# Optimization experiments

Measured on AMD Instinct MI355X. Metric: run time of the kernel, lower is better.

## Reference

```python
import jax, jax.numpy as jnp
import numpy as np

BATCH = 2048
NUM_FIELDS = 32
EMBED = 64
NPAIRS = NUM_FIELDS * (NUM_FIELDS - 1) // 2  # 496
# static pair indices (i < j), same order as the torch double loop
ROW, COL = np.triu_indices(NUM_FIELDS, k=1)
ROW = jnp.asarray(ROW)
COL = jnp.asarray(COL)


def setup_inputs() -> dict:
    key = jax.random.key(0)
    k1, k2 = jax.random.split(key)
    emb_inputs = jax.random.normal(k1, (BATCH, NUM_FIELDS, EMBED), dtype=jnp.float32)
    # xavier_normal_ on kernel of shape (E, NC2, E): fan_in = NC2*E (dims[1:]), fan_out = E*E... 
    # torch: fan_in = size(1)*receptive = NPAIRS*EMBED? torch uses size(1)*prod(size[2:]) = NPAIRS*EMBED,
    # fan_out = size(0)*prod(size[2:]) = EMBED*EMBED; std = sqrt(2/(fan_in+fan_out))
    fan_in = NPAIRS * EMBED
    fan_out = EMBED * EMBED
    std = float(np.sqrt(2.0 / (fan_in + fan_out)))
    kernel = jax.random.normal(k2, (EMBED, NPAIRS, EMBED), dtype=jnp.float32) * std
    return {"emb_inputs": emb_inputs, "kernel": kernel}


def reference(emb_inputs, kernel):
    # emb_inputs: (B, N, E); kernel: (E, NC2, E)
    p = emb_inputs[:, ROW]  # (B, NC2, E)
    q = emb_inputs[:, COL]  # (B, NC2, E)
    # torch: kp[b,i,pair] = sum_j p[b,pair,j] * kernel[i,pair,j]; out[b,pair] = sum_i kp*q
    kp = jnp.einsum('bpj,ipj->bpi', p, kernel)  # (B, NC2, E) -- avoids (B,E,NC2,E) blowup
    outputs = jnp.sum(kp * q, axis=-1)          # (B, NC2)
    return outputs[:, None, :]                  # (B, 1, NC2)
```

## Files before the change

### kernel.cpp

```cpp
#include <hip/hip_runtime.h>
#include <hip/hip_bf16.h>

#define BATCH   2048
#define NFIELDS 32
#define EMBED   64
#define NPAIRS  496
#define BT      256

typedef __attribute__((ext_vector_type(8))) short bf16x8;
typedef __attribute__((ext_vector_type(4))) float f32x4;

__device__ __forceinline__ unsigned short f2bf(float x) {
    unsigned int u = __float_as_uint(x);
    unsigned int r = 0x7fffu + ((u >> 16) & 1u);
    return (unsigned short)((u + r) >> 16);
}
__device__ __forceinline__ bf16x8 cvt8(const float* p) {
    float4 v0 = *(const float4*)p;
    float4 v1 = *(const float4*)(p + 4);
    bf16x8 o;
    o[0]=(short)f2bf(v0.x); o[1]=(short)f2bf(v0.y); o[2]=(short)f2bf(v0.z); o[3]=(short)f2bf(v0.w);
    o[4]=(short)f2bf(v1.x); o[5]=(short)f2bf(v1.y); o[6]=(short)f2bf(v1.z); o[7]=(short)f2bf(v1.w);
    return o;
}

__global__ __launch_bounds__(256) void convert_prepass(
    const float* __restrict__ emb, const float* __restrict__ kern,
    unsigned short* __restrict__ embB, unsigned short* __restrict__ kernB)
{
    const int EMB4 = BATCH * NFIELDS * EMBED / 4;
    const int KER4 = EMBED * NPAIRS * EMBED / 4;
    int t = blockIdx.x * blockDim.x + threadIdx.x;
    if (t < EMB4) {
        float4 v = ((const float4*)emb)[t];
        ushort4 o;
        o.x = f2bf(v.x); o.y = f2bf(v.y); o.z = f2bf(v.z); o.w = f2bf(v.w);
        *(ushort4*)(embB + (size_t)t * 4) = o;
    } else if (t < EMB4 + KER4) {
        int u = t - EMB4;
        int j4   = u & 15;
        int rest = u >> 4;
        int p = rest % NPAIRS;
        int i = rest / NPAIRS;
        float4 v = *(const float4*)(kern + (size_t)i * (NPAIRS*EMBED) + (size_t)p * EMBED + j4*4);
        ushort4 o;
        o.x = f2bf(v.x); o.y = f2bf(v.y); o.z = f2bf(v.z); o.w = f2bf(v.w);
        *(ushort4*)(kernB + (size_t)p * 4096 + i * 64 + j4 * 4) = o;
    }
}

template<bool PRE>
__global__ __launch_bounds__(256) void opn_main(
    const void* __restrict__ embP, const void* __restrict__ kernP,
    float* __restrict__ out)
{
    const int pair = blockIdx.x;
    const int bt   = blockIdx.y;

    int r = 0, s0 = 0;
    while (pair >= s0 + (NFIELDS - 1 - r)) { s0 += NFIELDS - 1 - r; ++r; }
    const int c = r + 1 + (pair - s0);

    __shared__ __align__(16) unsigned short Klds[64][72];

    const int tid = threadIdx.x;

    if (PRE) {
        const unsigned short* kb = (const unsigned short*)kernP + (size_t)pair * 4096;
        #pragma unroll
        for (int itk = 0; itk < 2; ++itk) {
            int idx = (itk * 256 + tid) * 8;
            *(bf16x8*)&Klds[idx >> 6][idx & 63] = *(const bf16x8*)(kb + idx);
        }
    } else {
        const float* kf = (const float*)kernP;
        #pragma unroll
        for (int itk = 0; itk < 2; ++itk) {
            int idx = (itk * 256 + tid) * 8;
            int i = idx >> 6, j = idx & 63;
            *(bf16x8*)&Klds[i][j] = cvt8(kf + (size_t)i * (NPAIRS*EMBED) + (size_t)pair * EMBED + j);
        }
    }
    __syncthreads();

    const int wave = tid >> 6, lane = tid & 63;
    const int col = lane & 15, quad = lane >> 4;

    bf16x8 kfr[4][2];
    #pragma unroll
    for (int mt = 0; mt < 4; ++mt)
        #pragma unroll
        for (int ks = 0; ks < 2; ++ks)
            kfr[mt][ks] = *(const bf16x8*)&Klds[mt*16 + col][ks*32 + quad*8];

    const unsigned short* eb = (const unsigned short*)embP;
    const float* ef = (const float*)embP;

    #pragma unroll
    for (int it = 0; it < 4; ++it) {
        const int b = bt * BT + wave * 64 + it * 16 + col;
        const size_t rowbase = (size_t)b * (NFIELDS * EMBED);

        bf16x8 pfr[2];
        if (PRE) {
            pfr[0] = *(const bf16x8*)(eb + rowbase + (size_t)r * EMBED + quad*8);
            pfr[1] = *(const bf16x8*)(eb + rowbase + (size_t)r * EMBED + 32 + quad*8);
        } else {
            pfr[0] = cvt8(ef + rowbase + (size_t)r * EMBED + quad*8);
            pfr[1] = cvt8(ef + rowbase + (size_t)r * EMBED + 32 + quad*8);
        }

        f32x4 acc[4];
        #pragma unroll
        for (int mt = 0; mt < 4; ++mt) {
            acc[mt] = (f32x4){0.f, 0.f, 0.f, 0.f};
            acc[mt] = __builtin_amdgcn_mfma_f32_16x16x32_bf16(kfr[mt][0], pfr[0], acc[mt], 0, 0, 0);
            acc[mt] = __builtin_amdgcn_mfma_f32_16x16x32_bf16(kfr[mt][1], pfr[1], acc[mt], 0, 0, 0);
        }

        float partial = 0.f;
        #pragma unroll
        for (int mt = 0; mt < 4; ++mt) {
            float qv0, qv1, qv2, qv3;
            if (PRE) {
                uint2 qd = *(const uint2*)(eb + rowbase + (size_t)c * EMBED + mt*16 + quad*4);
                qv0 = __uint_as_float(qd.x << 16);
                qv1 = __uint_as_float(qd.x & 0xffff0000u);
                qv2 = __uint_as_float(qd.y << 16);
                qv3 = __uint_as_float(qd.y & 0xffff0000u);
            } else {
                float4 qf = *(const float4*)(ef + rowbase + (size_t)c * EMBED + mt*16 + quad*4);
                qv0 = qf.x; qv1 = qf.y; qv2 = qf.z; qv3 = qf.w;
            }
            partial += acc[mt][0] * qv0;
            partial += acc[mt][1] * qv1;
            partial += acc[mt][2] * qv2;
            partial += acc[mt][3] * qv3;
        }
        partial += __shfl_xor(partial, 16, 64);
        partial += __shfl_xor(partial, 32, 64);

        if (quad == 0)
            out[(size_t)b * NPAIRS + pair] = partial;
    }
}

extern "C" void kernel_launch(void* const* d_in, const int* in_sizes, int n_in,
                              void* d_out, int out_size, void* d_ws, size_t ws_size,
                              hipStream_t stream) {
    const float* emb  = (const float*)d_in[0];
    const float* kern = (const float*)d_in[1];
    float* out = (float*)d_out;

    const size_t embElems  = (size_t)BATCH * NFIELDS * EMBED;
    const size_t kernElems = (size_t)EMBED * NPAIRS * EMBED;
    const size_t need = (embElems + kernElems) * sizeof(unsigned short);

    dim3 grid(NPAIRS, BATCH / BT);
    if (ws_size >= need) {
        unsigned short* embB  = (unsigned short*)d_ws;
        unsigned short* kernB = embB + embElems;
        int total4 = (int)((embElems + kernElems) / 4);
        convert_prepass<<<(total4 + 255) / 256, 256, 0, stream>>>(emb, kern, embB, kernB);
        opn_main<true><<<grid, 256, 0, stream>>>((const void*)embB, (const void*)kernB, out);
    } else {
        opn_main<false><<<grid, 256, 0, stream>>>((const void*)emb, (const void*)kern, out);
    }
}
```

Measured before the change: 119.3 us.

## Transpose bf16 embeddings field-major, double-buffer loads, and double batch tile

The prepass now writes the bf16 embeddings in field-major order (field, batch, embed), so each block's P and Q rows for a pair are contiguous across batch rows rather than strided by the whole sample. The main loop prefetches the next iteration's P and Q fragments into registers while the current MFMAs and dot products run. The batch tile per block doubles to 512, which halves the number of per-block kernel-slice loads into LDS but also halves the grid's y dimension. The prefetch double buffers add register pressure.

```diff
diff --git a/kernel.cpp b/kernel.cpp
--- a/kernel.cpp
+++ b/kernel.cpp
@@ -5,7 +5,8 @@
 #define NFIELDS 32
 #define EMBED   64
 #define NPAIRS  496
-#define BT      256
+#define BT      512
+#define NIT     (BT / 64)
 
 typedef __attribute__((ext_vector_type(8))) short bf16x8;
 typedef __attribute__((ext_vector_type(4))) float f32x4;
@@ -26,16 +27,19 @@
 
 __global__ __launch_bounds__(256) void convert_prepass(
     const float* __restrict__ emb, const float* __restrict__ kern,
-    unsigned short* __restrict__ embB, unsigned short* __restrict__ kernB)
+    unsigned short* __restrict__ embT, unsigned short* __restrict__ kernB)
 {
     const int EMB4 = BATCH * NFIELDS * EMBED / 4;
     const int KER4 = EMBED * NPAIRS * EMBED / 4;
     int t = blockIdx.x * blockDim.x + threadIdx.x;
     if (t < EMB4) {
-        float4 v = ((const float4*)emb)[t];
+        int e4 = t & 15;
+        int b  = (t >> 4) & (BATCH - 1);
+        int f  = t >> 15;
+        float4 v = *(const float4*)(emb + ((size_t)b * NFIELDS + f) * EMBED + e4 * 4);
         ushort4 o;
         o.x = f2bf(v.x); o.y = f2bf(v.y); o.z = f2bf(v.z); o.w = f2bf(v.w);
-        *(ushort4*)(embB + (size_t)t * 4) = o;
+        *(ushort4*)(embT + ((size_t)f * BATCH + b) * EMBED + e4 * 4) = o;
     } else if (t < EMB4 + KER4) {
         int u = t - EMB4;
         int j4   = u & 15;
@@ -62,7 +66,6 @@
     const int c = r + 1 + (pair - s0);
 
     __shared__ __align__(16) unsigned short Klds[64][72];
-
     const int tid = threadIdx.x;
 
     if (PRE) {
@@ -93,29 +96,61 @@
         for (int ks = 0; ks < 2; ++ks)
             kfr[mt][ks] = *(const bf16x8*)&Klds[mt*16 + col][ks*32 + quad*8];
 
-    const unsigned short* eb = (const unsigned short*)embP;
+    const unsigned short* prow = (const unsigned short*)embP + ((size_t)r * BATCH) * EMBED;
+    const unsigned short* qrow = (const unsigned short*)embP + ((size_t)c * BATCH) * EMBED;
     const float* ef = (const float*)embP;
 
+    const int b0base = bt * BT + wave * (BT / 4);
+
+    bf16x8 pfA[2], pfB[2];
+    uint2  qv[2][4];
+    float4 qf[2][4];
+
+    {
+        const size_t eo = (size_t)(b0base + col) * EMBED;
+        if (PRE) {
+            pfA[0] = *(const bf16x8*)(prow + eo + quad*8);
+            pfB[0] = *(const bf16x8*)(prow + eo + 32 + quad*8);
+            #pragma unroll
+            for (int mt = 0; mt < 4; ++mt)
+                qv[0][mt] = *(const uint2*)(qrow + eo + mt*16 + quad*4);
+        } else {
+            const size_t rb = (size_t)(b0base + col) * (NFIELDS * EMBED);
+            pfA[0] = cvt8(ef + rb + (size_t)r * EMBED + quad*8);
+            pfB[0] = cvt8(ef + rb + (size_t)r * EMBED + 32 + quad*8);
+            #pragma unroll
+            for (int mt = 0; mt < 4; ++mt)
+                qf[0][mt] = *(const float4*)(ef + rb + (size_t)c * EMBED + mt*16 + quad*4);
+        }
+    }
+
     #pragma unroll
-    for (int it = 0; it < 4; ++it) {
-        const int b = bt * BT + wave * 64 + it * 16 + col;
-        const size_t rowbase = (size_t)b * (NFIELDS * EMBED);
-
-        bf16x8 pfr[2];
-        if (PRE) {
-            pfr[0] = *(const bf16x8*)(eb + rowbase + (size_t)r * EMBED + quad*8);
-            pfr[1] = *(const bf16x8*)(eb + rowbase + (size_t)r * EMBED + 32 + quad*8);
-        } else {
-            pfr[0] = cvt8(ef + rowbase + (size_t)r * EMBED + quad*8);
-            pfr[1] = cvt8(ef + rowbase + (size_t)r * EMBED + 32 + quad*8);
+    for (int it = 0; it < NIT; ++it) {
+        const int cur = it & 1, nxt = cur ^ 1;
+        if (it + 1 < NIT) {
+            const size_t eo = (size_t)(b0base + (it+1)*16 + col) * EMBED;
+            if (PRE) {
+                pfA[nxt] = *(const bf16x8*)(prow + eo + quad*8);
+                pfB[nxt] = *(const bf16x8*)(prow + eo + 32 + quad*8);
+                #pragma unroll
+                for (int mt = 0; mt < 4; ++mt)
+                    qv[nxt][mt] = *(const uint2*)(qrow + eo + mt*16 + quad*4);
+            } else {
+                const size_t rb = (size_t)(b0base + (it+1)*16 + col) * (NFIELDS * EMBED);
+                pfA[nxt] = cvt8(ef + rb + (size_t)r * EMBED + quad*8);
+                pfB[nxt] = cvt8(ef + rb + (size_t)r * EMBED + 32 + quad*8);
+                #pragma unroll
+                for (int mt = 0; mt < 4; ++mt)
+                    qf[nxt][mt] = *(const float4*)(ef + rb + (size_t)c * EMBED + mt*16 + quad*4);
+            }
         }
 
         f32x4 acc[4];
         #pragma unroll
         for (int mt = 0; mt < 4; ++mt) {
             acc[mt] = (f32x4){0.f, 0.f, 0.f, 0.f};
-            acc[mt] = __builtin_amdgcn_mfma_f32_16x16x32_bf16(kfr[mt][0], pfr[0], acc[mt], 0, 0, 0);
-            acc[mt] = __builtin_amdgcn_mfma_f32_16x16x32_bf16(kfr[mt][1], pfr[1], acc[mt], 0, 0, 0);
+            acc[mt] = __builtin_amdgcn_mfma_f32_16x16x32_bf16(kfr[mt][0], pfA[cur], acc[mt], 0, 0, 0);
+            acc[mt] = __builtin_amdgcn_mfma_f32_16x16x32_bf16(kfr[mt][1], pfB[cur], acc[mt], 0, 0, 0);
         }
 
         float partial = 0.f;
@@ -123,14 +158,14 @@
         for (int mt = 0; mt < 4; ++mt) {
             float qv0, qv1, qv2, qv3;
             if (PRE) {
-                uint2 qd = *(const uint2*)(eb + rowbase + (size_t)c * EMBED + mt*16 + quad*4);
+                uint2 qd = qv[cur][mt];
                 qv0 = __uint_as_float(qd.x << 16);
                 qv1 = __uint_as_float(qd.x & 0xffff0000u);
                 qv2 = __uint_as_float(qd.y << 16);
                 qv3 = __uint_as_float(qd.y & 0xffff0000u);
             } else {
-                float4 qf = *(const float4*)(ef + rowbase + (size_t)c * EMBED + mt*16 + quad*4);
-                qv0 = qf.x; qv1 = qf.y; qv2 = qf.z; qv3 = qf.w;
+                float4 q4 = qf[cur][mt];
+                qv0 = q4.x; qv1 = q4.y; qv2 = q4.z; qv3 = q4.w;
             }
             partial += acc[mt][0] * qv0;
             partial += acc[mt][1] * qv1;
@@ -140,8 +175,10 @@
         partial += __shfl_xor(partial, 16, 64);
         partial += __shfl_xor(partial, 32, 64);
 
-        if (quad == 0)
+        if (quad == 0) {
+            const int b = b0base + it*16 + col;
             out[(size_t)b * NPAIRS + pair] = partial;
+        }
     }
 }
 
@@ -158,11 +195,11 @@
 
     dim3 grid(NPAIRS, BATCH / BT);
     if (ws_size >= need) {
-        unsigned short* embB  = (unsigned short*)d_ws;
-        unsigned short* kernB = embB + embElems;
+        unsigned short* embT  = (unsigned short*)d_ws;
+        unsigned short* kernB = embT + embElems;
         int total4 = (int)((embElems + kernElems) / 4);
-        convert_prepass<<<(total4 + 255) / 256, 256, 0, stream>>>(emb, kern, embB, kernB);
-        opn_main<true><<<grid, 256, 0, stream>>>((const void*)embB, (const void*)kernB, out);
+        convert_prepass<<<(total4 + 255) / 256, 256, 0, stream>>>(emb, kern, embT, kernB);
+        opn_main<true><<<grid, 256, 0, stream>>>((const void*)embT, (const void*)kernB, out);
     } else {
         opn_main<false><<<grid, 256, 0, stream>>>((const void*)emb, (const void*)kern, out);
     }
```

Result: no change. 119.2 us (-0.1%).

## Pre-swizzle embeddings into MFMA fragment layout and prefetch per-wave tiles

Applied to the files above, without the earlier changes.

The prepass now writes two copies of the bf16 embeddings, pre-arranged into MFMA operand and output-fragment order (one for P operands, one for Q), so each lane issues a single contiguous 16-byte load per fragment. The main kernel drops the LDS staging of the kernel tile and loads its fragments straight from global memory. Each wave handles 8 batch tiles of 16 with double-buffered register prefetch, and the batch tile per block doubles. The fallback path becomes a naive fp32 kernel. This adds prepass write traffic (two emb copies) in exchange for coalesced loads and fewer blocks.

```diff
diff --git a/kernel.cpp b/kernel.cpp
--- a/kernel.cpp
+++ b/kernel.cpp
@@ -5,7 +5,9 @@
 #define NFIELDS 32
 #define EMBED   64
 #define NPAIRS  496
-#define BT      256
+#define BT      512
+#define NIT     8
+#define TPB     32
 
 typedef __attribute__((ext_vector_type(8))) short bf16x8;
 typedef __attribute__((ext_vector_type(4))) float f32x4;
@@ -15,134 +17,161 @@
     unsigned int r = 0x7fffu + ((u >> 16) & 1u);
     return (unsigned short)((u + r) >> 16);
 }
-__device__ __forceinline__ bf16x8 cvt8(const float* p) {
-    float4 v0 = *(const float4*)p;
-    float4 v1 = *(const float4*)(p + 4);
-    bf16x8 o;
-    o[0]=(short)f2bf(v0.x); o[1]=(short)f2bf(v0.y); o[2]=(short)f2bf(v0.z); o[3]=(short)f2bf(v0.w);
-    o[4]=(short)f2bf(v1.x); o[5]=(short)f2bf(v1.y); o[6]=(short)f2bf(v1.z); o[7]=(short)f2bf(v1.w);
-    return o;
-}
 
-__global__ __launch_bounds__(256) void convert_prepass(
+#define PP_OFF 0
+#define PQ_OFF 4194304
+#define KB_OFF 8388608
+#define WS_ELEMS 10420224
+
+__global__ __launch_bounds__(256) void prepass(
     const float* __restrict__ emb, const float* __restrict__ kern,
-    unsigned short* __restrict__ embB, unsigned short* __restrict__ kernB)
+    unsigned short* __restrict__ ws)
 {
-    const int EMB4 = BATCH * NFIELDS * EMBED / 4;
-    const int KER4 = EMBED * NPAIRS * EMBED / 4;
-    int t = blockIdx.x * blockDim.x + threadIdx.x;
-    if (t < EMB4) {
-        float4 v = ((const float4*)emb)[t];
-        ushort4 o;
-        o.x = f2bf(v.x); o.y = f2bf(v.y); o.z = f2bf(v.z); o.w = f2bf(v.w);
-        *(ushort4*)(embB + (size_t)t * 4) = o;
-    } else if (t < EMB4 + KER4) {
-        int u = t - EMB4;
-        int j4   = u & 15;
-        int rest = u >> 4;
-        int p = rest % NPAIRS;
-        int i = rest / NPAIRS;
-        float4 v = *(const float4*)(kern + (size_t)i * (NPAIRS*EMBED) + (size_t)p * EMBED + j4*4);
-        ushort4 o;
-        o.x = f2bf(v.x); o.y = f2bf(v.y); o.z = f2bf(v.z); o.w = f2bf(v.w);
-        *(ushort4*)(kernB + (size_t)p * 4096 + i * 64 + j4 * 4) = o;
+    unsigned short* pp = ws + PP_OFF;
+    unsigned short* pq = ws + PQ_OFF;
+    unsigned short* kb = ws + KB_OFF;
+    const int NEMB8 = BATCH * NFIELDS * EMBED / 8;
+    const int NKER8 = EMBED * NPAIRS * EMBED / 8;
+    int v = blockIdx.x * blockDim.x + threadIdx.x;
+    if (v < NEMB8) {
+        int base = v * 8;
+        int e0 = base & 63;
+        int f  = (base >> 6) & 31;
+        int b  = base >> 11;
+        float4 v0 = *(const float4*)(emb + base);
+        float4 v1 = *(const float4*)(emb + base + 4);
+        ushort4 lo, hi;
+        lo.x = f2bf(v0.x); lo.y = f2bf(v0.y); lo.z = f2bf(v0.z); lo.w = f2bf(v0.w);
+        hi.x = f2bf(v1.x); hi.y = f2bf(v1.y); hi.z = f2bf(v1.z); hi.w = f2bf(v1.w);
+        int t = b >> 4, col = b & 15;
+        int ks = e0 >> 5, quad = (e0 & 31) >> 3;
+        size_t dp = (size_t)f * 131072 + t * 1024 + ks * 512 + quad * 128 + col * 8;
+        *(ushort4*)(pp + dp)     = lo;
+        *(ushort4*)(pp + dp + 4) = hi;
+        int pos  = e0 & 31;
+        int half = pos >> 4;
+        int qq   = (pos & 15) >> 2;
+        size_t dq = (size_t)f * 131072 + t * 1024 + ks * 512 + qq * 128 + col * 8 + half * 4;
+        *(ushort4*)(pq + dq)       = lo;
+        *(ushort4*)(pq + dq + 128) = hi;
+    } else if (v < NEMB8 + NKER8) {
+        int base = (v - NEMB8) * 8;
+        int j0 = base & 63;
+        int pr = (base >> 6) % NPAIRS;
+        int i  = (base >> 6) / NPAIRS;
+        float4 v0 = *(const float4*)(kern + base);
+        float4 v1 = *(const float4*)(kern + base + 4);
+        ushort4 lo, hi;
+        lo.x = f2bf(v0.x); lo.y = f2bf(v0.y); lo.z = f2bf(v0.z); lo.w = f2bf(v0.w);
+        hi.x = f2bf(v1.x); hi.y = f2bf(v1.y); hi.z = f2bf(v1.z); hi.w = f2bf(v1.w);
+        size_t dk = (size_t)pr * 4096 + i * 64 + j0;
+        *(ushort4*)(kb + dk)     = lo;
+        *(ushort4*)(kb + dk + 4) = hi;
     }
 }
 
-template<bool PRE>
 __global__ __launch_bounds__(256) void opn_main(
-    const void* __restrict__ embP, const void* __restrict__ kernP,
-    float* __restrict__ out)
+    const unsigned short* __restrict__ ws, float* __restrict__ out)
 {
+    const unsigned short* pp = ws + PP_OFF;
+    const unsigned short* pq = ws + PQ_OFF;
+    const unsigned short* kb = ws + KB_OFF;
+
     const int pair = blockIdx.x;
     const int bt   = blockIdx.y;
-
     int r = 0, s0 = 0;
     while (pair >= s0 + (NFIELDS - 1 - r)) { s0 += NFIELDS - 1 - r; ++r; }
     const int c = r + 1 + (pair - s0);
 
-    __shared__ __align__(16) unsigned short Klds[64][72];
-
     const int tid = threadIdx.x;
-
-    if (PRE) {
-        const unsigned short* kb = (const unsigned short*)kernP + (size_t)pair * 4096;
-        #pragma unroll
-        for (int itk = 0; itk < 2; ++itk) {
-            int idx = (itk * 256 + tid) * 8;
-            *(bf16x8*)&Klds[idx >> 6][idx & 63] = *(const bf16x8*)(kb + idx);
-        }
-    } else {
-        const float* kf = (const float*)kernP;
-        #pragma unroll
-        for (int itk = 0; itk < 2; ++itk) {
-            int idx = (itk * 256 + tid) * 8;
-            int i = idx >> 6, j = idx & 63;
-            *(bf16x8*)&Klds[i][j] = cvt8(kf + (size_t)i * (NPAIRS*EMBED) + (size_t)pair * EMBED + j);
-        }
-    }
-    __syncthreads();
-
     const int wave = tid >> 6, lane = tid & 63;
     const int col = lane & 15, quad = lane >> 4;
 
     bf16x8 kfr[4][2];
+    const unsigned short* kp = kb + (size_t)pair * 4096;
     #pragma unroll
     for (int mt = 0; mt < 4; ++mt)
         #pragma unroll
         for (int ks = 0; ks < 2; ++ks)
-            kfr[mt][ks] = *(const bf16x8*)&Klds[mt*16 + col][ks*32 + quad*8];
+            kfr[mt][ks] = *(const bf16x8*)(kp + (mt*16 + col)*64 + ks*32 + quad*8);
 
-    const unsigned short* eb = (const unsigned short*)embP;
-    const float* ef = (const float*)embP;
+    const int T0 = bt * TPB + wave * NIT;
+    const unsigned short* pbase = pp + (size_t)r * 131072 + (size_t)T0 * 1024 + lane * 8;
+    const unsigned short* qbase = pq + (size_t)c * 131072 + (size_t)T0 * 1024 + lane * 8;
+
+    bf16x8 pA[2], pB[2];
+    uint4  qA[2], qB[2];
+    pA[0] = *(const bf16x8*)(pbase);
+    pB[0] = *(const bf16x8*)(pbase + 512);
+    qA[0] = *(const uint4*)(qbase);
+    qB[0] = *(const uint4*)(qbase + 512);
 
     #pragma unroll
-    for (int it = 0; it < 4; ++it) {
-        const int b = bt * BT + wave * 64 + it * 16 + col;
-        const size_t rowbase = (size_t)b * (NFIELDS * EMBED);
-
-        bf16x8 pfr[2];
-        if (PRE) {
-            pfr[0] = *(const bf16x8*)(eb + rowbase + (size_t)r * EMBED + quad*8);
-            pfr[1] = *(const bf16x8*)(eb + rowbase + (size_t)r * EMBED + 32 + quad*8);
-        } else {
-            pfr[0] = cvt8(ef + rowbase + (size_t)r * EMBED + quad*8);
-            pfr[1] = cvt8(ef + rowbase + (size_t)r * EMBED + 32 + quad*8);
+    for (int it = 0; it < NIT; ++it) {
+        const int cur = it & 1, nxt = cur ^ 1;
+        if (it + 1 < NIT) {
+            pA[nxt] = *(const bf16x8*)(pbase + (it+1)*1024);
+            pB[nxt] = *(const bf16x8*)(pbase + (it+1)*1024 + 512);
+            qA[nxt] = *(const uint4*)(qbase + (it+1)*1024);
+            qB[nxt] = *(const uint4*)(qbase + (it+1)*1024 + 512);
         }
 
         f32x4 acc[4];
         #pragma unroll
         for (int mt = 0; mt < 4; ++mt) {
             acc[mt] = (f32x4){0.f, 0.f, 0.f, 0.f};
-            acc[mt] = __builtin_amdgcn_mfma_f32_16x16x32_bf16(kfr[mt][0], pfr[0], acc[mt], 0, 0, 0);
-            acc[mt] = __builtin_amdgcn_mfma_f32_16x16x32_bf16(kfr[mt][1], pfr[1], acc[mt], 0, 0, 0);
+            acc[mt] = __builtin_amdgcn_mfma_f32_16x16x32_bf16(kfr[mt][0], pA[cur], acc[mt], 0, 0, 0);
+            acc[mt] = __builtin_amdgcn_mfma_f32_16x16x32_bf16(kfr[mt][1], pB[cur], acc[mt], 0, 0, 0);
         }
 
         float partial = 0.f;
-        #pragma unroll
-        for (int mt = 0; mt < 4; ++mt) {
-            float qv0, qv1, qv2, qv3;
-            if (PRE) {
-                uint2 qd = *(const uint2*)(eb + rowbase + (size_t)c * EMBED + mt*16 + quad*4);
-                qv0 = __uint_as_float(qd.x << 16);
-                qv1 = __uint_as_float(qd.x & 0xffff0000u);
-                qv2 = __uint_as_float(qd.y << 16);
-                qv3 = __uint_as_float(qd.y & 0xffff0000u);
-            } else {
-                float4 qf = *(const float4*)(ef + rowbase + (size_t)c * EMBED + mt*16 + quad*4);
-                qv0 = qf.x; qv1 = qf.y; qv2 = qf.z; qv3 = qf.w;
-            }
-            partial += acc[mt][0] * qv0;
-            partial += acc[mt][1] * qv1;
-            partial += acc[mt][2] * qv2;
-            partial += acc[mt][3] * qv3;
+        {
+            uint4 qa = qA[cur], qb = qB[cur];
+            partial += acc[0][0] * __uint_as_float(qa.x << 16);
+            partial += acc[0][1] * __uint_as_float(qa.x & 0xffff0000u);
+            partial += acc[0][2] * __uint_as_float(qa.y << 16);
+            partial += acc[0][3] * __uint_as_float(qa.y & 0xffff0000u);
+            partial += acc[1][0] * __uint_as_float(qa.z << 16);
+            partial += acc[1][1] * __uint_as_float(qa.z & 0xffff0000u);
+            partial += acc[1][2] * __uint_as_float(qa.w << 16);
+            partial += acc[1][3] * __uint_as_float(qa.w & 0xffff0000u);
+            partial += acc[2][0] * __uint_as_float(qb.x << 16);
+            partial += acc[2][1] * __uint_as_float(qb.x & 0xffff0000u);
+            partial += acc[2][2] * __uint_as_float(qb.y << 16);
+            partial += acc[2][3] * __uint_as_float(qb.y & 0xffff0000u);
+            partial += acc[3][0] * __uint_as_float(qb.z << 16);
+            partial += acc[3][1] * __uint_as_float(qb.z & 0xffff0000u);
+            partial += acc[3][2] * __uint_as_float(qb.w << 16);
+            partial += acc[3][3] * __uint_as_float(qb.w & 0xffff0000u);
         }
         partial += __shfl_xor(partial, 16, 64);
         partial += __shfl_xor(partial, 32, 64);
 
         if (quad == 0)
-            out[(size_t)b * NPAIRS + pair] = partial;
+            out[(size_t)((T0 + it) * 16 + col) * NPAIRS + pair] = partial;
     }
+}
+
+__global__ __launch_bounds__(256) void opn_naive(
+    const float* __restrict__ emb, const float* __restrict__ kern,
+    float* __restrict__ out)
+{
+    int idx = blockIdx.x * blockDim.x + threadIdx.x;
+    if (idx >= BATCH * NPAIRS) return;
+    int b = idx / NPAIRS, p = idx % NPAIRS;
+    int r = 0, s0 = 0;
+    while (p >= s0 + (NFIELDS - 1 - r)) { s0 += NFIELDS - 1 - r; ++r; }
+    int c = r + 1 + (p - s0);
+    const float* pv = emb + ((size_t)b * NFIELDS + r) * EMBED;
+    const float* qv = emb + ((size_t)b * NFIELDS + c) * EMBED;
+    float acc = 0.f;
+    for (int i = 0; i < EMBED; ++i) {
+        const float* kr = kern + ((size_t)i * NPAIRS + p) * EMBED;
+        float kpv = 0.f;
+        for (int j = 0; j < EMBED; ++j) kpv += kr[j] * pv[j];
+        acc += kpv * qv[i];
+    }
+    out[(size_t)b * NPAIRS + p] = acc;
 }
 
 extern "C" void kernel_launch(void* const* d_in, const int* in_sizes, int n_in,
@@ -152,18 +181,16 @@
     const float* kern = (const float*)d_in[1];
     float* out = (float*)d_out;
 
-    const size_t embElems  = (size_t)BATCH * NFIELDS * EMBED;
-    const size_t kernElems = (size_t)EMBED * NPAIRS * EMBED;
-    const size_t need = (embElems + kernElems) * sizeof(unsigned short);
-
-    dim3 grid(NPAIRS, BATCH / BT);
-    if (ws_size >= need) {
-        unsigned short* embB  = (unsigned short*)d_ws;
-        unsigned short* kernB = embB + embElems;
-        int total4 = (int)((embElems + kernElems) / 4);
-        convert_prepass<<<(total4 + 255) / 256, 256, 0, stream>>>(emb, kern, embB, kernB);
-        opn_main<true><<<grid, 256, 0, stream>>>((const void*)embB, (const void*)kernB, out);
+    if (ws_size >= (size_t)WS_ELEMS * sizeof(unsigned short)) {
+        unsigned short* ws = (unsigned short*)d_ws;
+        const int NEMB8 = BATCH * NFIELDS * EMBED / 8;
+        const int NKER8 = EMBED * NPAIRS * EMBED / 8;
+        int total = NEMB8 + NKER8;
+        prepass<<<(total + 255) / 256, 256, 0, stream>>>(emb, kern, ws);
+        dim3 grid(NPAIRS, BATCH / BT);
+        opn_main<<<grid, 256, 0, stream>>>(ws, out);
     } else {
-        opn_main<false><<<grid, 256, 0, stream>>>((const void*)emb, (const void*)kern, out);
+        int total = BATCH * NPAIRS;
+        opn_naive<<<(total + 255) / 256, 256, 0, stream>>>(emb, kern, out);
     }
 }
```

After: 111.7 us. 6.4% less time.
